# Kernel optimization log

Measured on AMD Instinct MI355X. Metric: run time of the kernel, lower is better.

The kernel has to match this reference:

```python
import jax, jax.numpy as jnp
import numpy as np

B, N, D, Q, H = 8, 2048, 64, 16, 2
C = 2 * D + 1          # combined dim = 129
C8 = C // 8            # per-head qk dim = 16
K = 8192               # number of observed nodes
NEG = -9.0e15


def setup_inputs() -> dict:
    key = jax.random.key(0)
    ks = jax.random.split(key, 18)
    s = 0.05
    inp = {
        "x": jax.random.normal(ks[0], (B, N, D + 1), jnp.float32),
        "h": jax.random.normal(ks[1], (B, N, D), jnp.float32),
        "query_vectors": jax.random.normal(ks[2], (K, Q), jnp.float32),
        "adj": jax.random.randint(ks[3], (B, N, N), 0, 2, jnp.int32),
        "nodes_flat": jnp.arange(K, dtype=jnp.int32),
        # per-head attention projections (jax convention: x @ W + b)
        "Wq": jax.random.normal(ks[4], (H, C, C8), jnp.float32) * s,
        "bq": jax.random.normal(ks[5], (H, C8), jnp.float32) * s,
        "Wk": jax.random.normal(ks[6], (H, C, C8), jnp.float32) * s,
        "bk": jax.random.normal(ks[7], (H, C8), jnp.float32) * s,
        "Wv": jax.random.normal(ks[8], (H, C, C), jnp.float32) * s,
        "bv": jax.random.normal(ks[9], (H, C), jnp.float32) * s,
        # hypernetwork MLP_Param weights for reset / update / candidate gates
        "W_r": jax.random.normal(ks[10], (Q, C, D), jnp.float32) * s,
        "b_r": jax.random.normal(ks[11], (Q, D), jnp.float32) * s,
        "W_u": jax.random.normal(ks[12], (Q, C, D), jnp.float32) * s,
        "b_u": jax.random.normal(ks[13], (Q, D), jnp.float32) * s,
        "W_c": jax.random.normal(ks[14], (Q, C, D), jnp.float32) * s,
        "b_c": jax.random.normal(ks[15], (Q, D), jnp.float32) * s,
    }
    return inp


def _gate(x_sel, qv, W, b):
    # MLP_Param: W_n = einsum('nd,dio->nio', qv, W); out = x @ W_n + qv @ b
    # contract the combined dim first to avoid the [K, C, D] intermediate
    t = jnp.einsum('kc,qco->kqo', x_sel, W)      # [K, Q, D]
    return jnp.einsum('kq,kqo->ko', qv, t) + qv @ b


def reference(x, h, query_vectors, adj, nodes_flat,
              Wq, bq, Wk, bk, Wv, bv,
              W_r, b_r, W_u, b_u, W_c, b_c):
    combined = jnp.concatenate([x, h], axis=-1)                 # [B, N, C]
    q = jnp.einsum('bnc,hcd->hbnd', combined, Wq) + bq[:, None, None, :]
    k = jnp.einsum('bnc,hcd->hbnd', combined, Wk) + bk[:, None, None, :]
    v = jnp.einsum('bnc,hcd->hbnd', combined, Wv) + bv[:, None, None, :]
    scores = jnp.einsum('hbnd,hbmd->hbnm', q, k) / jnp.sqrt(jnp.float32(C8))
    scores = jax.nn.leaky_relu(scores, 0.2)
    scores = jnp.where(adj[None] == 0, NEG, scores)
    attn = jax.nn.softmax(scores, axis=-1)                      # [H, B, N, N]
    h_prime = jnp.einsum('hbnm,hbmc->hbnc', attn, v)
    comb_attn = h_prime.mean(axis=0)                            # [B, N, C]

    sel = comb_attn.reshape(-1, C)[nodes_flat]                  # [K, C]
    r = jax.nn.sigmoid(_gate(sel, query_vectors, W_r, b_r))     # [K, D]
    u = jax.nn.sigmoid(_gate(sel, query_vectors, W_u, b_u))     # [K, D]

    h_flat = h.reshape(-1, D)
    h_sel = r * h_flat[nodes_flat]                              # r * h[nodes_ind]
    h_flat = h_flat.at[nodes_flat].set(h_sel)
    h_new = h_flat.reshape(h.shape)

    comb_new = jnp.concatenate([x, h_new], axis=-1)             # [B, N, C]
    sel2 = comb_new.reshape(-1, C)[nodes_flat]
    cand = jnp.tanh(_gate(sel2, query_vectors, W_c, b_c))       # [K, D]

    return (1.0 - u) * h_sel + u * cand                         # [K, D]
```

## Files before the change

kernel.cpp:

```cpp
#include <hip/hip_runtime.h>
#include <hip/hip_bf16.h>


typedef _Float16 h2_t __attribute__((ext_vector_type(2)));
typedef _Float16 h8_t __attribute__((ext_vector_type(8)));
typedef float    f4_t __attribute__((ext_vector_type(4)));
#define MFMA16x32(a,b,c) __builtin_amdgcn_mfma_f32_16x16x32_f16(a,b,c,0,0,0)

#define OB_QG    0
#define OB_KG    524288
#define OB_VT    1048576
#define OB_MASK  5767168
#define OB_WALL  7864320
#define OB_HACC  7971840
#define OB_LSUM  16622592
#define OB_WTRU  16688128
#define OB_WTC   17253376

__global__ __launch_bounds__(256) void pack_adj(const int* __restrict__ adj,
                                                unsigned* __restrict__ mask) {
    long tg = (long)blockIdx.x * 256 + threadIdx.x;
    for (int it = 0; it < 32; ++it) {
        long i = tg + (long)it * 524288;
        int a = adj[i];
        unsigned long long bal = __ballot(a != 0);
        if ((threadIdx.x & 63) == 0)
            *(unsigned long long*)(mask + (i >> 5)) = bal;
    }
}

__global__ __launch_bounds__(256) void repack_all(
    const float* __restrict__ Wq, const float* __restrict__ bq,
    const float* __restrict__ Wk, const float* __restrict__ bk,
    const float* __restrict__ Wv, const float* __restrict__ bv,
    const float* __restrict__ Wr, const float* __restrict__ br,
    const float* __restrict__ Wu, const float* __restrict__ bu,
    const float* __restrict__ Wc, const float* __restrict__ bc,
    _Float16* __restrict__ Wall, _Float16* __restrict__ WtRu,
    _Float16* __restrict__ WtC) {
    int idx = blockIdx.x * 256 + threadIdx.x;
    if (idx < 6720) {
        int ct = idx / 320;
        int rem = idx % 320;
        int s = rem >> 6, lane = rem & 63;
        int n = ct * 16 + (lane & 15);
        int quad = lane >> 4;
        int h2 = (n >= 164) ? 1 : 0;
        int nn = n - h2 * 164;
        h8_t v;
        #pragma unroll
        for (int j = 0; j < 8; ++j) {
            int k = s * 32 + quad * 8 + j;
            float f = 0.f;
            if (n < 328) {
                if (nn < 16) {
                    if (k < 129)       f = Wq[(h2 * 129 + k) * 16 + nn];
                    else if (k == 129) f = bq[h2 * 16 + nn];
                } else if (nn < 32) {
                    int d = nn - 16;
                    if (k < 129)       f = Wk[(h2 * 129 + k) * 16 + d];
                    else if (k == 129) f = bk[h2 * 16 + d];
                } else {
                    int vc = nn - 32;
                    if (vc < 129) {
                        if (k < 129)       f = Wv[(h2 * 129 + k) * 129 + vc];
                        else if (k == 129) f = bv[h2 * 129 + vc];
                    }
                }
            }
            v[j] = (_Float16)f;
        }
        *(h8_t*)(Wall + (size_t)idx * 8) = v;
    } else if (idx < 6720 + 35328) {
        int i2 = idx - 6720;
        int s = i2 / 512;
        int rem = i2 % 512;
        int ct = rem >> 6, lane = rem & 63;
        int o = ct * 16 + (lane & 15);
        int quad = lane >> 4;
        const float* W = (o < 64) ? Wr : Wu;
        const float* bb = (o < 64) ? br : bu;
        int oc = o & 63;
        h8_t v;
        #pragma unroll
        for (int j = 0; j < 8; ++j) {
            int kk = s * 32 + quad * 8 + j;
            float f = 0.f;
            if (kk < 2176) {
                int q = kk / 136, c = kk % 136;
                if (c < 129) f = W[(q * 129 + c) * 64 + oc];
            } else if (kk < 2192) {
                f = bb[(kk - 2176) * 64 + oc];
            }
            v[j] = (_Float16)f;
        }
        *(h8_t*)(WtRu + (size_t)i2 * 8) = v;
    } else if (idx < 59712) {
        int i2 = idx - 6720 - 35328;
        int s = i2 / 256;
        int rem = i2 % 256;
        int ct = rem >> 6, lane = rem & 63;
        int o = ct * 16 + (lane & 15);
        int quad = lane >> 4;
        h8_t v;
        #pragma unroll
        for (int j = 0; j < 8; ++j) {
            int kk = s * 32 + quad * 8 + j;
            float f = 0.f;
            if (kk < 2176) {
                int q = kk / 136, c = kk % 136;
                if (c < 129) f = Wc[(q * 129 + c) * 64 + o];
            } else if (kk < 2192) {
                f = bc[(kk - 2176) * 64 + o];
            }
            v[j] = (_Float16)f;
        }
        *(h8_t*)(WtC + (size_t)i2 * 8) = v;
    }
}

__global__ __launch_bounds__(256) void qkv_mfma(
    const float* __restrict__ x, const float* __restrict__ h,
    const _Float16* __restrict__ Wall,
    _Float16* __restrict__ qg, _Float16* __restrict__ kg,
    _Float16* __restrict__ vT) {
    __shared__ _Float16 at[16 * 168];
    __shared__ _Float16 vls[264 * 16];
    int t = threadIdx.x;
    int row0 = blockIdx.x * 16;
    for (int idx = t; idx < 16 * 160; idx += 256) {
        int r = idx / 160, c = idx % 160;
        int grow = row0 + r;
        float v = 0.f;
        if (c < 65)       v = x[grow * 65 + c];
        else if (c < 129) v = h[grow * 64 + (c - 65)];
        else if (c == 129) v = 1.0f;
        at[r * 168 + c] = (_Float16)v;
    }
    __syncthreads();
    int lane = t & 63, w = t >> 6;
    int l16 = lane & 15, quad = lane >> 4;
    for (int ct = w; ct < 21; ct += 4) {
        f4_t acc; acc[0]=0.f; acc[1]=0.f; acc[2]=0.f; acc[3]=0.f;
        int n = ct * 16 + l16;
        const _Float16* wp = Wall + ((size_t)ct * 320 + lane) * 8;
        #pragma unroll
        for (int s = 0; s < 5; ++s) {
            h8_t a = *(const h8_t*)(at + l16 * 168 + s * 32 + quad * 8);
            h8_t b = *(const h8_t*)(wp + (size_t)s * 512);
            acc = MFMA16x32(a, b, acc);
        }
        if (n < 328) {
            int h2 = (n >= 164) ? 1 : 0;
            int nn = n - h2 * 164;
            #pragma unroll
            for (int r = 0; r < 4; ++r) {
                int row = quad * 4 + r;
                _Float16 v = (_Float16)acc[r];
                if (nn < 16)      qg[(h2 * 8192 + row0 + row) * 16 + nn] = v;
                else if (nn < 32) kg[(h2 * 8192 + row0 + row) * 16 + (nn - 16)] = v;
                else              vls[(h2 * 132 + (nn - 32)) * 16 + row] = v;
            }
        }
    }
    __syncthreads();
    for (int idx = t; idx < 528; idx += 256) {
        int col = idx >> 1, half = idx & 1;
        int h2 = (col >= 132) ? 1 : 0;
        int cc = col - h2 * 132;
        uint4 v = ((const uint4*)vls)[idx];
        *(uint4*)(vT + ((size_t)(h2 * 144 + cc)) * 8192 + row0 + half * 8) = v;
    }
}

__global__ __launch_bounds__(256) void attn_fused(
    const _Float16* __restrict__ qg, const _Float16* __restrict__ kg,
    const _Float16* __restrict__ vT, const unsigned* __restrict__ mask,
    float* __restrict__ hacc, float* __restrict__ lsum, int tps) {
    __shared__ _Float16 vsm[144 * 64];
    __shared__ _Float16 pT[4 * 16 * 88];
    int t = threadIdx.x;
    int pid = blockIdx.x + 32 * (blockIdx.y + 8 * blockIdx.z);
    int xcd = pid & 7, j = pid >> 3;
    int nt = j & 31, hb = xcd, sp = j >> 5;
    int h2 = hb >> 2, b = hb & 3;
    int base = h2 * 8192 + b * 2048;
    int n0 = nt * 64;
    int lane = t & 63, w = t >> 6;
    int l16 = lane & 15, q = lane >> 4;
    int qrow = n0 + w * 16 + l16;
    _Float16* pTw = pT + w * 16 * 88;
    h8_t zero8;
    #pragma unroll
    for (int i = 0; i < 8; ++i) zero8[i] = (_Float16)0.f;
    h8_t qf = zero8;
    if (q < 2) qf = *(const h8_t*)(qg + (base + qrow) * 16 + 8 * q);
    const unsigned* mrw = mask + (b * 2048 + qrow) * 64;
    f4_t acc[9];
    #pragma unroll
    for (int i = 0; i < 9; ++i) { acc[i][0]=0.f; acc[i][1]=0.f; acc[i][2]=0.f; acc[i][3]=0.f; }
    float l_run = 0.f;

    int vcol_l = (lane >> 3);
    int kch_l  = (lane & 7) ^ vcol_l;
    const _Float16* vtb = vT + (size_t)h2 * 144 * 8192 + b * 2048 + 8 * kch_l;
    int mt0 = sp * tps, mtE = sp * tps + tps;

    h8_t kpre[4];
    uint2 mpre;
    {
        int m0 = mt0 * 64;
        for (int jj = w; jj < 18; jj += 4)
            __builtin_amdgcn_global_load_lds(
                (const void*)(vtb + (size_t)(8 * jj + vcol_l) * 8192 + m0),
                (void*)(vsm + jj * 512), 16, 0, 0);
        #pragma unroll
        for (int ct = 0; ct < 4; ++ct) {
            kpre[ct] = zero8;
            if (q < 2)
                kpre[ct] = *(const h8_t*)(kg + (base + m0 + 16 * ct + l16) * 16 + 8 * q);
        }
        mpre = *(const uint2*)(mrw + (m0 >> 5));
    }

    for (int mt = mt0; mt < mtE; ++mt) {
        h8_t kf[4];
        #pragma unroll
        for (int ct = 0; ct < 4; ++ct) kf[ct] = kpre[ct];
        uint2 mw = mpre;
        f4_t st[4];
        #pragma unroll
        for (int ct = 0; ct < 4; ++ct) {
            f4_t z4; z4[0]=0.f; z4[1]=0.f; z4[2]=0.f; z4[3]=0.f;
            st[ct] = MFMA16x32(kf[ct], qf, z4);
        }
        #pragma unroll
        for (int ct = 0; ct < 4; ++ct) {
            unsigned wb = (ct < 2) ? mw.x : mw.y;
            float p[4];
            #pragma unroll
            for (int r = 0; r < 4; ++r) {
                float sc = st[ct][r] * 0.25f;
                sc = sc > 0.f ? sc : 0.2f * sc;
                int bit = ((ct & 1) ? 16 : 0) + 4 * q + r;
                p[r] = ((wb >> bit) & 1u) ? __expf(sc) : 0.f;
                l_run += p[r];
            }
            h2_t p01; p01[0] = (_Float16)p[0]; p01[1] = (_Float16)p[1];
            h2_t p23; p23[0] = (_Float16)p[2]; p23[1] = (_Float16)p[3];
            *(h2_t*)(pTw + l16 * 88 + 16 * ct + 4 * q)     = p01;
            *(h2_t*)(pTw + l16 * 88 + 16 * ct + 4 * q + 2) = p23;
        }
        __syncthreads();
        if (mt + 1 < mtE) {
            int m1 = (mt + 1) * 64;
            #pragma unroll
            for (int ct = 0; ct < 4; ++ct) {
                kpre[ct] = zero8;
                if (q < 2)
                    kpre[ct] = *(const h8_t*)(kg + (base + m1 + 16 * ct + l16) * 16 + 8 * q);
            }
            mpre = *(const uint2*)(mrw + (m1 >> 5));
        }
        const char* vbb = (const char*)vsm;
        __builtin_amdgcn_s_setprio(1);
        #pragma unroll
        for (int kh = 0; kh < 2; ++kh) {
            h8_t ap = *(const h8_t*)(pTw + l16 * 88 + 32 * kh + 8 * q);
            int xsw = (((kh << 2) + q) ^ (l16 & 7)) << 4;
            #pragma unroll
            for (int nb = 0; nb < 9; ++nb) {
                h8_t vf = *(const h8_t*)(vbb + ((16 * nb + l16) << 7) + xsw);
                acc[nb] = MFMA16x32(ap, vf, acc[nb]);
            }
        }
        __builtin_amdgcn_s_setprio(0);
        __syncthreads();
        if (mt + 1 < mtE) {
            int m1 = (mt + 1) * 64;
            for (int jj = w; jj < 18; jj += 4)
                __builtin_amdgcn_global_load_lds(
                    (const void*)(vtb + (size_t)(8 * jj + vcol_l) * 8192 + m1),
                    (void*)(vsm + jj * 512), 16, 0, 0);
        }
    }
    l_run += __shfl_xor(l_run, 16);
    l_run += __shfl_xor(l_run, 32);
    float* hc = hacc + (size_t)h2 * 8192 * 132;
    if (q == 0)
        atomicAdd(lsum + h2 * 8192 + b * 2048 + n0 + w * 16 + l16, l_run);
    #pragma unroll
    for (int nb = 0; nb < 9; ++nb) {
        int vc = 16 * nb + l16;
        if (vc < 132) {
            #pragma unroll
            for (int r = 0; r < 4; ++r) {
                int grow = b * 2048 + n0 + w * 16 + 4 * q + r;
                atomicAdd(hc + grow * 132 + vc, acc[nb][r]);
            }
        }
    }
}

__global__ __launch_bounds__(256) void gate_fused(
    const float* __restrict__ hacc, const float* __restrict__ lsum,
    const int* __restrict__ nodes, const float* __restrict__ qv,
    const _Float16* __restrict__ WtRu, const _Float16* __restrict__ WtC,
    const float* __restrict__ hbuf, const float* __restrict__ x,
    float* __restrict__ out) {
    __shared__ _Float16 selh[16 * 152];
    __shared__ _Float16 selh2[16 * 152];
    __shared__ float qvs[16 * 17];
    __shared__ float invl[32];
    __shared__ float hslds[16 * 66];
    __shared__ float ulds[16 * 66];
    int t = threadIdx.x;
    int k0 = blockIdx.x * 16;
    if (t < 32) {
        int r = t >> 1, hh = t & 1;
        int grow = nodes[k0 + r];
        invl[t] = 0.5f / lsum[hh * 8192 + grow];
    }
    __syncthreads();
    for (int idx = t; idx < 16 * 136; idx += 256) {
        int r = idx / 136, c = idx % 136;
        _Float16 v = (_Float16)0.f;
        if (c < 132) {
            int grow = nodes[k0 + r];
            v = (_Float16)(hacc[grow * 132 + c] * invl[r * 2] +
                           hacc[8192 * 132 + grow * 132 + c] * invl[r * 2 + 1]);
        }
        selh[r * 152 + c] = v;
    }
    for (int idx = t; idx < 16 * 136; idx += 256) {
        int r = idx / 136, c = idx % 136;
        _Float16 v = (_Float16)0.f;
        if (c < 65) v = (_Float16)x[nodes[k0 + r] * 65 + c];
        selh2[r * 152 + c] = v;
    }
    if (t < 256) {
        int r = t >> 4, q = t & 15;
        qvs[r * 17 + q] = qv[(k0 + r) * 16 + q];
    }
    __syncthreads();
    int lane = t & 63, w = t >> 6;
    int l16 = lane & 15, quad = lane >> 4;
    f4_t acc0, acc1;
    acc0[0]=0.f;acc0[1]=0.f;acc0[2]=0.f;acc0[3]=0.f;
    acc1[0]=0.f;acc1[1]=0.f;acc1[2]=0.f;acc1[3]=0.f;
    const _Float16* wp0 = WtRu + ((size_t)(2 * w) * 64 + lane) * 8;
    const _Float16* wp1 = wp0 + 512;
    for (int step = 0; step < 69; ++step) {
        h8_t a;
        if (step < 68) {
            int chunk = 4 * step + quad;
            int q = chunk / 17;
            int c0 = (chunk - q * 17) * 8;
            h8_t s8 = *(const h8_t*)(selh + l16 * 152 + c0);
            _Float16 qh = (_Float16)qvs[l16 * 17 + q];
            #pragma unroll
            for (int j = 0; j < 8; ++j) a[j] = s8[j] * qh;
        } else {
            int kl = quad * 8;
            #pragma unroll
            for (int j = 0; j < 8; ++j) {
                int kq = kl + j;
                a[j] = (kq < 16) ? (_Float16)qvs[l16 * 17 + kq] : (_Float16)0.f;
            }
        }
        h8_t b0 = *(const h8_t*)(wp0 + (size_t)step * 4096);
        h8_t b1 = *(const h8_t*)(wp1 + (size_t)step * 4096);
        acc0 = MFMA16x32(a, b0, acc0);
        acc1 = MFMA16x32(a, b1, acc1);
    }
    #pragma unroll
    for (int tt = 0; tt < 2; ++tt) {
        f4_t ac = tt ? acc1 : acc0;
        int o = (2 * w + tt) * 16 + l16;
        #pragma unroll
        for (int r = 0; r < 4; ++r) {
            int row = quad * 4 + r;
            float sg = 1.f / (1.f + __expf(-ac[r]));
            if (o < 64) {
                float hs = sg * hbuf[nodes[k0 + row] * 64 + o];
                hslds[row * 66 + o] = hs;
                selh2[row * 152 + 65 + o] = (_Float16)hs;
            } else {
                ulds[row * 66 + (o - 64)] = sg;
            }
        }
    }
    if (t < 112) {
        int r = t / 7, c = 129 + (t % 7);
        selh2[r * 152 + c] = (_Float16)0.f;
    }
    __syncthreads();
    f4_t acc2;
    acc2[0]=0.f;acc2[1]=0.f;acc2[2]=0.f;acc2[3]=0.f;
    const _Float16* wp = WtC + ((size_t)w * 64 + lane) * 8;
    for (int step = 0; step < 69; ++step) {
        h8_t a;
        if (step < 68) {
            int chunk = 4 * step + quad;
            int q = chunk / 17;
            int c0 = (chunk - q * 17) * 8;
            h8_t s8 = *(const h8_t*)(selh2 + l16 * 152 + c0);
            _Float16 qh = (_Float16)qvs[l16 * 17 + q];
            #pragma unroll
            for (int j = 0; j < 8; ++j) a[j] = s8[j] * qh;
        } else {
            int kl = quad * 8;
            #pragma unroll
            for (int j = 0; j < 8; ++j) {
                int kq = kl + j;
                a[j] = (kq < 16) ? (_Float16)qvs[l16 * 17 + kq] : (_Float16)0.f;
            }
        }
        h8_t b = *(const h8_t*)(wp + (size_t)step * 2048);
        acc2 = MFMA16x32(a, b, acc2);
    }
    int o = w * 16 + l16;
    #pragma unroll
    for (int r = 0; r < 4; ++r) {
        int row = quad * 4 + r;
        float cv = tanhf(acc2[r]);
        float hs = hslds[row * 66 + o];
        float uv = ulds[row * 66 + o];
        out[(k0 + row) * 64 + o] = (1.f - uv) * hs + uv * cv;
    }
}

extern "C" void kernel_launch(void* const* d_in, const int* in_sizes, int n_in,
                              void* d_out, int out_size, void* d_ws, size_t ws_size,
                              hipStream_t stream) {
    const float* x   = (const float*)d_in[0];
    const float* h   = (const float*)d_in[1];
    const float* qv  = (const float*)d_in[2];
    const int*   adj = (const int*)d_in[3];
    const int*   nod = (const int*)d_in[4];
    const float* Wq  = (const float*)d_in[5];
    const float* bq  = (const float*)d_in[6];
    const float* Wk  = (const float*)d_in[7];
    const float* bk  = (const float*)d_in[8];
    const float* Wv  = (const float*)d_in[9];
    const float* bv  = (const float*)d_in[10];
    const float* Wr  = (const float*)d_in[11];
    const float* br  = (const float*)d_in[12];
    const float* Wu  = (const float*)d_in[13];
    const float* bu  = (const float*)d_in[14];
    const float* Wc  = (const float*)d_in[15];
    const float* bc  = (const float*)d_in[16];

    char* wsb = (char*)d_ws;
    _Float16* qg   = (_Float16*)(wsb + OB_QG);
    _Float16* kg   = (_Float16*)(wsb + OB_KG);
    _Float16* vT   = (_Float16*)(wsb + OB_VT);
    unsigned* mask = (unsigned*)(wsb + OB_MASK);
    _Float16* Wall = (_Float16*)(wsb + OB_WALL);
    float* hacc    = (float*)(wsb + OB_HACC);
    float* lsum    = (float*)(wsb + OB_LSUM);
    _Float16* WtRu = (_Float16*)(wsb + OB_WTRU);
    _Float16* WtC  = (_Float16*)(wsb + OB_WTC);

    pack_adj<<<dim3(2048), 256, 0, stream>>>(adj, mask);
    repack_all<<<dim3(234), 256, 0, stream>>>(Wq, bq, Wk, bk, Wv, bv,
                                              Wr, br, Wu, bu, Wc, bc,
                                              Wall, WtRu, WtC);
    qkv_mfma<<<dim3(512), 256, 0, stream>>>(x, h, Wall, qg, kg, vT);
    hipMemsetAsync(hacc, 0, (size_t)8650752 + 65536, stream);
    attn_fused<<<dim3(32, 8, 4), 256, 0, stream>>>(qg, kg, vT, mask,
                                                   hacc, lsum, 8);
    gate_fused<<<dim3(512), 256, 0, stream>>>(hacc, lsum, nod, qv,
                                              WtRu, WtC, h, x,
                                              (float*)d_out);
}
```

Before: 344.9 us.

## Drop split-K in attention, double-buffer V tiles, write results without atomics

The attention kernel no longer splits the key dimension four ways. Each block now walks all 32 key tiles for its query tile, so partial outputs and row sums are stored directly instead of accumulated with atomicAdd, and the memset of the accumulation buffer is gone. V tiles are double-buffered in LDS so the next tile's load can overlap the current tile's MFMA work, removing one barrier per iteration. The cost is a four-times smaller grid: 256 blocks, roughly one per CU, which reduces occupancy and the latency hiding that came from having many resident blocks.

```diff
diff --git a/kernel.cpp b/kernel.cpp
--- a/kernel.cpp
+++ b/kernel.cpp
@@ -176,13 +176,12 @@
 __global__ __launch_bounds__(256) void attn_fused(
     const _Float16* __restrict__ qg, const _Float16* __restrict__ kg,
     const _Float16* __restrict__ vT, const unsigned* __restrict__ mask,
-    float* __restrict__ hacc, float* __restrict__ lsum, int tps) {
-    __shared__ _Float16 vsm[144 * 64];
+    float* __restrict__ hacc, float* __restrict__ lsum, int ntiles) {
+    __shared__ _Float16 vsm[2 * 144 * 64];
     __shared__ _Float16 pT[4 * 16 * 88];
     int t = threadIdx.x;
-    int pid = blockIdx.x + 32 * (blockIdx.y + 8 * blockIdx.z);
-    int xcd = pid & 7, j = pid >> 3;
-    int nt = j & 31, hb = xcd, sp = j >> 5;
+    int pid = blockIdx.x + 32 * blockIdx.y;
+    int hb = pid & 7, nt = pid >> 3;
     int h2 = hb >> 2, b = hb & 3;
     int base = h2 * 8192 + b * 2048;
     int n0 = nt * 64;
@@ -204,26 +203,23 @@
     int vcol_l = (lane >> 3);
     int kch_l  = (lane & 7) ^ vcol_l;
     const _Float16* vtb = vT + (size_t)h2 * 144 * 8192 + b * 2048 + 8 * kch_l;
-    int mt0 = sp * tps, mtE = sp * tps + tps;
 
     h8_t kpre[4];
     uint2 mpre;
-    {
-        int m0 = mt0 * 64;
-        for (int jj = w; jj < 18; jj += 4)
-            __builtin_amdgcn_global_load_lds(
-                (const void*)(vtb + (size_t)(8 * jj + vcol_l) * 8192 + m0),
-                (void*)(vsm + jj * 512), 16, 0, 0);
-        #pragma unroll
-        for (int ct = 0; ct < 4; ++ct) {
-            kpre[ct] = zero8;
-            if (q < 2)
-                kpre[ct] = *(const h8_t*)(kg + (base + m0 + 16 * ct + l16) * 16 + 8 * q);
-        }
-        mpre = *(const uint2*)(mrw + (m0 >> 5));
-    }
-
-    for (int mt = mt0; mt < mtE; ++mt) {
+    for (int jj = w; jj < 18; jj += 4)
+        __builtin_amdgcn_global_load_lds(
+            (const void*)(vtb + (size_t)(8 * jj + vcol_l) * 8192),
+            (void*)(vsm + jj * 512), 16, 0, 0);
+    #pragma unroll
+    for (int ct = 0; ct < 4; ++ct) {
+        kpre[ct] = zero8;
+        if (q < 2)
+            kpre[ct] = *(const h8_t*)(kg + (base + 16 * ct + l16) * 16 + 8 * q);
+    }
+    mpre = *(const uint2*)mrw;
+
+    for (int mt = 0; mt < ntiles; ++mt) {
+        int cur = mt & 1;
         h8_t kf[4];
         #pragma unroll
         for (int ct = 0; ct < 4; ++ct) kf[ct] = kpre[ct];
@@ -251,8 +247,7 @@
             *(h2_t*)(pTw + l16 * 88 + 16 * ct + 4 * q)     = p01;
             *(h2_t*)(pTw + l16 * 88 + 16 * ct + 4 * q + 2) = p23;
         }
-        __syncthreads();
-        if (mt + 1 < mtE) {
+        if (mt + 1 < ntiles) {
             int m1 = (mt + 1) * 64;
             #pragma unroll
             for (int ct = 0; ct < 4; ++ct) {
@@ -262,33 +257,33 @@
             }
             mpre = *(const uint2*)(mrw + (m1 >> 5));
         }
-        const char* vbb = (const char*)vsm;
-        __builtin_amdgcn_s_setprio(1);
-        #pragma unroll
-        for (int kh = 0; kh < 2; ++kh) {
-            h8_t ap = *(const h8_t*)(pTw + l16 * 88 + 32 * kh + 8 * q);
-            int xsw = (((kh << 2) + q) ^ (l16 & 7)) << 4;
-            #pragma unroll
-            for (int nb = 0; nb < 9; ++nb) {
-                h8_t vf = *(const h8_t*)(vbb + ((16 * nb + l16) << 7) + xsw);
-                acc[nb] = MFMA16x32(ap, vf, acc[nb]);
-            }
-        }
-        __builtin_amdgcn_s_setprio(0);
         __syncthreads();
-        if (mt + 1 < mtE) {
+        if (mt + 1 < ntiles) {
             int m1 = (mt + 1) * 64;
             for (int jj = w; jj < 18; jj += 4)
                 __builtin_amdgcn_global_load_lds(
                     (const void*)(vtb + (size_t)(8 * jj + vcol_l) * 8192 + m1),
-                    (void*)(vsm + jj * 512), 16, 0, 0);
-        }
+                    (void*)(vsm + (cur ^ 1) * 9216 + jj * 512), 16, 0, 0);
+        }
+        const char* vbb = (const char*)(vsm + cur * 9216);
+        __builtin_amdgcn_s_setprio(1);
+        #pragma unroll
+        for (int kh = 0; kh < 2; ++kh) {
+            h8_t ap = *(const h8_t*)(pTw + l16 * 88 + 32 * kh + 8 * q);
+            int xsw = (((kh << 2) + q) ^ (l16 & 7)) << 4;
+            #pragma unroll
+            for (int nb = 0; nb < 9; ++nb) {
+                h8_t vf = *(const h8_t*)(vbb + ((16 * nb + l16) << 7) + xsw);
+                acc[nb] = MFMA16x32(ap, vf, acc[nb]);
+            }
+        }
+        __builtin_amdgcn_s_setprio(0);
     }
     l_run += __shfl_xor(l_run, 16);
     l_run += __shfl_xor(l_run, 32);
     float* hc = hacc + (size_t)h2 * 8192 * 132;
     if (q == 0)
-        atomicAdd(lsum + h2 * 8192 + b * 2048 + n0 + w * 16 + l16, l_run);
+        lsum[h2 * 8192 + b * 2048 + n0 + w * 16 + l16] = l_run;
     #pragma unroll
     for (int nb = 0; nb < 9; ++nb) {
         int vc = 16 * nb + l16;
@@ -296,7 +291,7 @@
             #pragma unroll
             for (int r = 0; r < 4; ++r) {
                 int grow = b * 2048 + n0 + w * 16 + 4 * q + r;
-                atomicAdd(hc + grow * 132 + vc, acc[nb][r]);
+                hc[grow * 132 + vc] = acc[nb][r];
             }
         }
     }
@@ -467,9 +462,8 @@
                                               Wr, br, Wu, bu, Wc, bc,
                                               Wall, WtRu, WtC);
     qkv_mfma<<<dim3(512), 256, 0, stream>>>(x, h, Wall, qg, kg, vT);
-    hipMemsetAsync(hacc, 0, (size_t)8650752 + 65536, stream);
-    attn_fused<<<dim3(32, 8, 4), 256, 0, stream>>>(qg, kg, vT, mask,
-                                                   hacc, lsum, 8);
+    attn_fused<<<dim3(32, 8, 1), 256, 0, stream>>>(qg, kg, vT, mask,
+                                                   hacc, lsum, 32);
     gate_fused<<<dim3(512), 256, 0, stream>>>(hacc, lsum, nod, qv,
                                               WtRu, WtC, h, x,
                                               (float*)d_out);
```

Result: faster. 322.7 us (-6.4%).
